# Kernel optimization log

Hardware: AMD Instinct MI355X
Metric: run time of the kernel (lower is better)

## Reference

```python
import jax, jax.numpy as jnp
import numpy as np

E, B, T, DIN, D = 8, 16, 512, 256, 256  # ensemble, batch, seq, input_dim, d_model*factor


def setup_inputs() -> dict:
    key = jax.random.key(0)
    ks = jax.random.split(key, 9)
    s_in = 1.0 / np.sqrt(DIN)
    s_d = 1.0 / np.sqrt(D)
    return {
        "x": jax.random.normal(ks[0], (E, B, T, DIN), jnp.float32),
        "hidden": jnp.zeros((1, E * B, 2 * D), jnp.float32),
        "rnn_start": (jax.random.uniform(ks[1], (B, T, 1)) < 0.02).astype(jnp.float32),
        "W_in": jax.random.normal(ks[2], (2, E, DIN, D), jnp.float32) * s_in,
        "b_in": jax.random.normal(ks[3], (2, E, D), jnp.float32) * 0.01,
        "W_mid": jax.random.normal(ks[4], (4, E, D, D), jnp.float32) * s_d,
        "b_mid": jax.random.normal(ks[5], (4, E, D), jnp.float32) * 0.01,
        "W_out": jax.random.normal(ks[6], (E, D, D), jnp.float32) * s_d,
        "b_out": jax.random.normal(ks[7], (E, D), jnp.float32) * 0.01,
    }


def _scan_tie_input_gate(v, f, h0):
    # h_t = f_t * h_{t-1} + (1 - f_t) * v_t  (tied input gate), via associative scan.
    # v, f: [N, T, D]; h0: [N, 1, D]
    b = (1.0 - f) * v

    def combine(x, y):
        a1, b1 = x
        a2, b2 = y
        return a1 * a2, a2 * b1 + b2

    A, Bc = jax.lax.associative_scan(combine, (f, b), axis=1)
    out = A * h0 + Bc  # [N, T, D]
    return out, out[:, -1:, :]


def reference(x, hidden, rnn_start, W_in, b_in, W_mid, b_mid, W_out, b_out):
    # --- first GILR stage ---
    u = jnp.einsum('ebti,meio->mebto', x, W_in) + b_in[:, :, None, None, :]
    v = jnp.tanh(u[0])
    f = jax.nn.sigmoid(u[1])
    f = f * (1.0 - rnn_start)[None]  # rnn_start [B,T,1] broadcasts over E, D

    vr = v.reshape(E * B, T, D)
    fr = f.reshape(E * B, T, D)

    h_pre, h_mid = jnp.split(hidden, 2, axis=-1)          # each [1, E*B, D]
    h_pre = jnp.transpose(h_pre, (1, 0, 2))               # [E*B, 1, D]
    h_mid = jnp.transpose(h_mid, (1, 0, 2))

    vr, h_pre_last = _scan_tie_input_gate(vr, fr, h_pre)
    v4 = vr.reshape(E, B, T, D)

    # --- LSTM-like middle stage ---
    u = jnp.einsum('ebti,meio->mebto', v4, W_mid) + b_mid[:, :, None, None, :]
    f = jax.nn.sigmoid(u[0])
    i = jax.nn.sigmoid(u[1])
    o = jax.nn.sigmoid(u[2])
    z = jnp.tanh(u[3])
    f = f * (1.0 - rnn_start)[None]

    fr = f.reshape(E * B, T, D)
    izr = (i * z).reshape(E * B, T, D)
    orr = o.reshape(E * B, T, D)

    out, h_mid_last = _scan_tie_input_gate(izr, fr, h_mid)
    out = out * orr
    out4 = out.reshape(E, B, T, D)

    # --- output projection ---
    out4 = jnp.einsum('ebti,eio->ebto', out4, W_out) + b_out[:, None, None, :]

    hidden_out = jnp.transpose(jnp.concatenate([h_pre_last, h_mid_last], axis=-1), (1, 0, 2))
    return out4, hidden_out
```

## Files before the change

### kernel.cpp

```cpp
#include <hip/hip_runtime.h>
#include <hip/hip_bf16.h>
#include <stdint.h>
#include <stddef.h>


typedef __bf16 bf16x8 __attribute__((ext_vector_type(8)));
typedef __bf16 bf16x4 __attribute__((ext_vector_type(4)));
typedef __bf16 bf16x2 __attribute__((ext_vector_type(2)));
typedef float  f32x4  __attribute__((ext_vector_type(4)));
typedef float  f32x2  __attribute__((ext_vector_type(2)));

#define E_ 8
#define M_ 8192
#define K_ 256

__device__ __forceinline__ float sigm_f(float x) {
    return __builtin_amdgcn_rcpf(1.0f + __expf(-x));
}
__device__ __forceinline__ float tanh_f(float x) {
    return 1.0f - 2.0f * __builtin_amdgcn_rcpf(1.0f + __expf(2.0f * x));
}

__device__ __forceinline__ void g2lds16(const void* g, void* l) {
    __builtin_amdgcn_global_load_lds((const __attribute__((address_space(1))) void*)g,
                                     (__attribute__((address_space(3))) void*)l, 16, 0, 0);
}

template <int D>
__device__ __forceinline__ float dppshr(float x) {
    return __builtin_bit_cast(float,
        __builtin_amdgcn_update_dpp(0, __builtin_bit_cast(int, x),
                                    0x110 | D, 0xF, 0xF, true));
}

__device__ __forceinline__ void lane_scan(float& A, float& B, float& EA, float& EB, int ln15) {
    float As, Bs;
    Bs = dppshr<1>(B); As = dppshr<1>(A); B = __builtin_fmaf(A, Bs, B); A = (ln15 >= 1) ? A * As : A;
    Bs = dppshr<2>(B); As = dppshr<2>(A); B = __builtin_fmaf(A, Bs, B); A = (ln15 >= 2) ? A * As : A;
    Bs = dppshr<4>(B); As = dppshr<4>(A); B = __builtin_fmaf(A, Bs, B); A = (ln15 >= 4) ? A * As : A;
    Bs = dppshr<8>(B); As = dppshr<8>(A); B = __builtin_fmaf(A, Bs, B); A = (ln15 >= 8) ? A * As : A;
    EA = dppshr<1>(A); EA = (ln15 >= 1) ? EA : 1.0f;
    EB = dppshr<1>(B);
}

__global__ __launch_bounds__(256) void transw_all(const float* __restrict__ W_in,
                                                  const float* __restrict__ W_mid,
                                                  const float* __restrict__ W_out,
                                                  __bf16* __restrict__ Wt1,
                                                  __bf16* __restrict__ Wt2,
                                                  __bf16* __restrict__ Wt3) {
    int z = blockIdx.z;
    const float* src; __bf16* dst; int NG, ilv, ge;
    if (z < 16)      { src = W_in;  dst = Wt1; NG = 2; ilv = 1; ge = z; }
    else if (z < 48) { src = W_mid; dst = Wt2; NG = 4; ilv = 1; ge = z - 16; }
    else             { src = W_out; dst = Wt3; NG = 1; ilv = 0; ge = z - 48; }
    int g = ge >> 3, e = ge & 7;
    int k0 = blockIdx.x * 64, d0 = blockIdx.y * 64;
    __shared__ float tile[64][65];
    int t = threadIdx.x;
#pragma unroll
    for (int j = 0; j < 16; ++j) {
        int lin = j * 256 + t;
        int r = lin >> 6, c = lin & 63;
        tile[r][c] = src[((size_t)(ge * 256 + k0 + r)) * 256 + d0 + c];
    }
    __syncthreads();
#pragma unroll
    for (int j = 0; j < 16; ++j) {
        int lin = j * 256 + t;
        int r = lin >> 6, c = lin & 63;
        int d = d0 + r;
        int row = ilv ? (d * NG + g) : (g * 256 + d);
        dst[((size_t)(e * NG * 256 + row)) * K_ + k0 + c] = (__bf16)tile[c][r];
    }
}

template <int MODE, int NG>
__global__ __launch_bounds__(512, 1) void gemm_k(const __bf16* __restrict__ A,
                                                 const float* __restrict__ Af,
                                                 const __bf16* __restrict__ Wt,
                                                 const float* __restrict__ bias,
                                                 const float* __restrict__ rs,
                                                 __bf16* __restrict__ gout,
                                                 float* __restrict__ fout,
                                                 const float* __restrict__ hidden,
                                                 float* __restrict__ hidout) {
    constexpr int NT  = NG * 2;
    constexpr int NMT = 2 * NT;
    const int tid = threadIdx.x;
    const int bid = blockIdx.x;
    const int e  = bid & 7;
    const int rr = bid >> 3;
    const int nt = rr & (NT - 1);
    const int ms = rr / NT;
    const int mt0 = ms * NMT;
    const int lane = tid & 63, wid = tid >> 6;
    const int wr = wid >> 2, wc = wid & 3;
    const int ln15 = lane & 15, ln16 = lane >> 4;

    __shared__ __align__(16) __bf16 As[2][32768];
    __shared__ float cAl[64], cBl[64];
    __shared__ float chL[2][64];

    bf16x8 Breg[2][8];
    {
        const __bf16* bp = Wt + ((size_t)e * (NG * 256) + nt * 128 + wc * 32 + ln15) * K_ + ln16 * 8;
#pragma unroll
        for (int j = 0; j < 2; ++j)
#pragma unroll
            for (int s = 0; s < 8; ++s)
                Breg[j][s] = *(const bf16x8*)(bp + (size_t)j * 16 * K_ + s * 32);
    }
    f32x4 bias_v[2];
#pragma unroll
    for (int j = 0; j < 2; ++j) {
        int n0 = nt * 128 + wc * 32 + j * 16 + (ln16 << 2);
        if constexpr (MODE == 0) {
#pragma unroll
            for (int q = 0; q < 4; ++q) {
                int n = n0 + q;
                bias_v[j][q] = bias[((n & 1) * E_ + e) * 256 + (n >> 1)];
            }
        } else if constexpr (MODE == 1) {
#pragma unroll
            for (int q = 0; q < 4; ++q) {
                int n = n0 + q;
                bias_v[j][q] = bias[((n & 3) * E_ + e) * 256 + (n >> 2)];
            }
        } else {
            bias_v[j] = *(const f32x4*)&bias[e * 256 + n0];
        }
    }

    const int sr = tid >> 5, sr2 = sr >> 2;
    const int gg0 = (tid & 31) ^ sr2;
    const size_t Aoff = ((size_t)e * M_ + (size_t)mt0 * 128) * K_;
    const __bf16* sE = nullptr; const __bf16* sO = nullptr;
    const float*  sEf = nullptr; const float* sOf = nullptr;
    if constexpr (MODE == 0) {
        sEf = Af + Aoff + (size_t)sr * K_ + gg0 * 8;
        sOf = Af + Aoff + (size_t)sr * K_ + (gg0 ^ 4) * 8;
    } else {
        sE = A + Aoff + (size_t)sr * K_ + gg0 * 8;
        sO = A + Aoff + (size_t)sr * K_ + (gg0 ^ 4) * 8;
    }
    __bf16* const dbase0 = &As[0][tid * 8];
    __bf16* const dbase1 = &As[1][tid * 8];

    auto stage = [&](int tt, int buf) {
        __bf16* d = buf ? dbase1 : dbase0;
        const size_t toff = (size_t)tt * (128 * K_);
#pragma unroll
        for (int q = 0; q < 8; ++q)
            g2lds16(((q & 1) ? sO : sE) + toff + q * (16 * K_), d + q * 4096);
    };

    f32x4 tA[8], tB[8];
    auto loadx = [&](int tt) {
        const size_t toff = (size_t)tt * (128 * K_);
#pragma unroll
        for (int q = 0; q < 8; ++q) {
            const float* s = ((q & 1) ? sOf : sEf) + toff + q * (16 * K_);
            tA[q] = *(const f32x4*)s;
            tB[q] = *(const f32x4*)(s + 4);
        }
    };
    auto writex = [&](int buf) {
        __bf16* d = buf ? dbase1 : dbase0;
#pragma unroll
        for (int q = 0; q < 8; ++q) {
            bf16x8 w;
#pragma unroll
            for (int k = 0; k < 4; ++k) { w[k] = (__bf16)tA[q][k]; w[4 + k] = (__bf16)tB[q][k]; }
            *(bf16x8*)(d + q * 4096) = w;
        }
    };

    const int rowb = (wr * 64 + ln15 * 4) * K_;
    const int gb = ln16 ^ (lane & 7);
    const int pe_off = rowb + gb * 8;
    const int po_off = rowb + (gb ^ 4) * 8;

    auto compute = [&](f32x4 (&acc)[4][2], int buf) {
        const __bf16* pe = &As[0][0] + buf * 32768 + pe_off;
        const __bf16* po = &As[0][0] + buf * 32768 + po_off;
#pragma unroll
        for (int s = 0; s < 8; ++s) {
            const __bf16* p = (s & 1) ? po : pe;
            bf16x8 af[4];
#pragma unroll
            for (int i = 0; i < 4; ++i)
                af[i] = *(const bf16x8*)(p + i * K_ + (s >> 1) * 64);
#pragma unroll
            for (int i = 0; i < 4; ++i)
#pragma unroll
                for (int j = 0; j < 2; ++j)
                    acc[i][j] = __builtin_amdgcn_mfma_f32_16x16x32_bf16(Breg[j][s], af[i], acc[i][j], 0, 0, 0);
        }
    };

    if constexpr (MODE == 2) {
        stage(0, 0);
        asm volatile("s_waitcnt vmcnt(0)" ::: "memory");
        __builtin_amdgcn_s_barrier();
        __builtin_amdgcn_sched_barrier(0);
        f32x4 acc[4][2] = {};
        int buf = 0;
        for (int t = 0; t < NMT; ++t) {
            if (t + 1 < NMT) stage(t + 1, buf ^ 1);
            compute(acc, buf);
            const int mb = (mt0 + t) * 128 + wr * 64 + ln15 * 4;
#pragma unroll
            for (int j = 0; j < 2; ++j) {
                const int n0 = nt * 128 + wc * 32 + j * 16 + (ln16 << 2);
#pragma unroll
                for (int i = 0; i < 4; ++i) {
                    f32x4 o = acc[i][j] + bias_v[j];
                    *(f32x4*)&fout[((size_t)e * M_ + mb + i) * 256 + n0] = o;
                    acc[i][j] = f32x4{};
                }
            }
            asm volatile("s_waitcnt vmcnt(8) lgkmcnt(0)" ::: "memory");
            __builtin_amdgcn_s_barrier();
            __builtin_amdgcn_sched_barrier(0);
            buf ^= 1;
        }
        return;
    } else {
        auto do_epi = [&](f32x4 (&acc)[4][2], int tp, const f32x4& rs4p, const float* hidvp) {
            const bool cs = ((tp & 3) == 0);
            const int c = tp >> 2;
            const int mb = (mt0 + tp) * 128 + wr * 64 + ln15 * 4;
            f32x4 rsv;
#pragma unroll
            for (int q = 0; q < 4; ++q) rsv[q] = 1.0f - rs4p[q];

            if constexpr (MODE == 1) {
                float PA[2][4], PB[2][4], Ov[2][4], LA[2], LB[2], EA[2], EB[2];
#pragma unroll
                for (int j = 0; j < 2; ++j) {
#pragma unroll
                    for (int i = 0; i < 4; ++i) {
                        float f  = sigm_f(acc[i][j][0] + bias_v[j][0]) * rsv[i];
                        float iv = sigm_f(acc[i][j][1] + bias_v[j][1]);
                        float o  = sigm_f(acc[i][j][2] + bias_v[j][2]);
                        float z  = tanh_f(acc[i][j][3] + bias_v[j][3]);
                        float b  = (1.0f - f) * iv * z;
                        Ov[j][i] = o;
                        if (i == 0) { PA[j][0] = f; PB[j][0] = b; }
                        else { PB[j][i] = __builtin_fmaf(f, PB[j][i - 1], b); PA[j][i] = PA[j][i - 1] * f; }
                        acc[i][j] = f32x4{};
                    }
                    LA[j] = PA[j][3]; LB[j] = PB[j][3];
                    lane_scan(LA[j], LB[j], EA[j], EB[j], ln15);
                }
                if (wr == 0 && ln15 == 15) {
#pragma unroll
                    for (int j = 0; j < 2; ++j) {
                        int sl = wc * 8 + j * 4 + ln16;
                        cAl[sl] = LA[j]; cBl[sl] = LB[j];
                    }
                }
                asm volatile("s_waitcnt lgkmcnt(0)" ::: "memory");
                __builtin_amdgcn_s_barrier();
#pragma unroll
                for (int j = 0; j < 2; ++j) {
                    const int sl = wc * 8 + j * 4 + ln16;
                    const int d = nt * 32 + wc * 8 + j * 4 + ln16;
                    float hp = cs ? hidvp[j] : chL[tp & 1][sl];
                    float hs = wr ? __builtin_fmaf(cAl[sl], hp, cBl[sl]) : hp;
                    float h0 = __builtin_fmaf(EA[j], hs, EB[j]);
#pragma unroll
                    for (int i = 0; i < 4; ++i) {
                        float h = __builtin_fmaf(PA[j][i], h0, PB[j][i]);
                        gout[((size_t)e * M_ + mb + i) * 256 + d] = (__bf16)(h * Ov[j][i]);
                    }
                    if (wr == 1 && ln15 == 15) {
                        float he = __builtin_fmaf(LA[j], hs, LB[j]);
                        chL[(tp + 1) & 1][sl] = he;
                        if ((tp & 3) == 3)
                            hidout[(e * 16 + ms * 4 + c) * 512 + 256 + d] = he;
                    }
                }
            } else {
                float PA[2][2][4], PB[2][2][4], LA[2][2], LB[2][2], EA[2][2], EB[2][2];
#pragma unroll
                for (int j = 0; j < 2; ++j) {
#pragma unroll
                    for (int dq = 0; dq < 2; ++dq) {
#pragma unroll
                        for (int i = 0; i < 4; ++i) {
                            float uv = acc[i][j][dq * 2 + 0] + bias_v[j][dq * 2 + 0];
                            float uf = acc[i][j][dq * 2 + 1] + bias_v[j][dq * 2 + 1];
                            float f = sigm_f(uf) * rsv[i];
                            float b = (1.0f - f) * tanh_f(uv);
                            if (i == 0) { PA[j][dq][0] = f; PB[j][dq][0] = b; }
                            else { PB[j][dq][i] = __builtin_fmaf(f, PB[j][dq][i - 1], b);
                                   PA[j][dq][i] = PA[j][dq][i - 1] * f; }
                        }
                        LA[j][dq] = PA[j][dq][3]; LB[j][dq] = PB[j][dq][3];
                        lane_scan(LA[j][dq], LB[j][dq], EA[j][dq], EB[j][dq], ln15);
                    }
#pragma unroll
                    for (int i = 0; i < 4; ++i) acc[i][j] = f32x4{};
                }
                if (wr == 0 && ln15 == 15) {
#pragma unroll
                    for (int j = 0; j < 2; ++j)
#pragma unroll
                        for (int dq = 0; dq < 2; ++dq) {
                            int sl = wc * 16 + j * 8 + ln16 * 2 + dq;
                            cAl[sl] = LA[j][dq]; cBl[sl] = LB[j][dq];
                        }
                }
                asm volatile("s_waitcnt lgkmcnt(0)" ::: "memory");
                __builtin_amdgcn_s_barrier();
#pragma unroll
                for (int j = 0; j < 2; ++j) {
                    const int D0 = nt * 64 + wc * 16 + j * 8 + ln16 * 2;
                    float h0q[2];
#pragma unroll
                    for (int dq = 0; dq < 2; ++dq) {
                        const int sl = wc * 16 + j * 8 + ln16 * 2 + dq;
                        float hp = cs ? hidvp[j * 2 + dq] : chL[tp & 1][sl];
                        float hs = wr ? __builtin_fmaf(cAl[sl], hp, cBl[sl]) : hp;
                        h0q[dq] = __builtin_fmaf(EA[j][dq], hs, EB[j][dq]);
                        if (wr == 1 && ln15 == 15) {
                            float he = __builtin_fmaf(LA[j][dq], hs, LB[j][dq]);
                            chL[(tp + 1) & 1][sl] = he;
                            if ((tp & 3) == 3)
                                hidout[(e * 16 + ms * 2 + c) * 512 + D0 + dq] = he;
                        }
                    }
#pragma unroll
                    for (int i = 0; i < 4; ++i) {
                        float ha = __builtin_fmaf(PA[j][0][i], h0q[0], PB[j][0][i]);
                        float hb = __builtin_fmaf(PA[j][1][i], h0q[1], PB[j][1][i]);
                        bf16x2 pk; pk[0] = (__bf16)ha; pk[1] = (__bf16)hb;
                        *(unsigned int*)&gout[((size_t)e * M_ + mb + i) * 256 + D0] =
                            __builtin_bit_cast(unsigned int, pk);
                    }
                }
            }
        };

        if constexpr (MODE == 0) {
            loadx(0);
            asm volatile("s_waitcnt vmcnt(0)" ::: "memory");
            writex(0);
            asm volatile("s_waitcnt lgkmcnt(0)" ::: "memory");
        } else {
            stage(0, 0);
            asm volatile("s_waitcnt vmcnt(0)" ::: "memory");
        }
        __builtin_amdgcn_s_barrier();
        __builtin_amdgcn_sched_barrier(0);

        f32x4 accA[4][2] = {}, accB[4][2] = {};
        f32x4 rs4_p = {};
        float hidv_p[4] = {0.f, 0.f, 0.f, 0.f};
        int buf = 0;

        auto iter = [&](int t, f32x4 (&accC)[4][2], f32x4 (&accP)[4][2]) {
            const int c = t >> 2;
            f32x4 rs4_n;
            float hidv_n[4] = {0.f, 0.f, 0.f, 0.f};
            {
                const int mbh = (mt0 + t) * 128 + wr * 64 + ln15 * 4;
                rs4_n = *(const f32x4*)&rs[mbh];
                if constexpr (MODE == 1) {
                    const int nrow = e * 16 + ms * 4 + c;
                    hidv_n[0] = hidden[nrow * 512 + 256 + (nt * 32 + wc * 8 + 0 + ln16)];
                    hidv_n[1] = hidden[nrow * 512 + 256 + (nt * 32 + wc * 8 + 4 + ln16)];
                } else {
                    const int nrow = e * 16 + ms * 2 + c;
                    f32x2 ha = *(const f32x2*)&hidden[nrow * 512 + (nt * 64 + wc * 16 + 0 + ln16 * 2)];
                    f32x2 hb = *(const f32x2*)&hidden[nrow * 512 + (nt * 64 + wc * 16 + 8 + ln16 * 2)];
                    hidv_n[0] = ha[0]; hidv_n[1] = ha[1]; hidv_n[2] = hb[0]; hidv_n[3] = hb[1];
                }
                __builtin_amdgcn_sched_barrier(0);
            }
            if constexpr (MODE == 0) {
                if (t + 1 < NMT) loadx(t + 1);
                __builtin_amdgcn_sched_barrier(0);
            } else {
                if (t + 1 < NMT) stage(t + 1, buf ^ 1);
            }
            compute(accC, buf);
            if (t > 0) do_epi(accP, t - 1, rs4_p, hidv_p);
            if (t == 0) {
                asm volatile("s_waitcnt vmcnt(0)" ::: "memory");
            } else {
                asm volatile("s_waitcnt vmcnt(8)" ::: "memory");
            }
            if constexpr (MODE == 0) {
                if (t + 1 < NMT) writex(buf ^ 1);
            }
            asm volatile("s_waitcnt lgkmcnt(0)" ::: "memory");
            __builtin_amdgcn_s_barrier();
            __builtin_amdgcn_sched_barrier(0);
            buf ^= 1;
            rs4_p = rs4_n;
#pragma unroll
            for (int q = 0; q < 4; ++q) hidv_p[q] = hidv_n[q];
        };

#pragma unroll 1
        for (int t2 = 0; t2 < NMT; t2 += 2) {
            iter(t2, accA, accB);
            iter(t2 + 1, accB, accA);
        }
        do_epi(accB, NMT - 1, rs4_p, hidv_p);
    }
}

extern "C" void kernel_launch(void* const* d_in, const int* in_sizes, int n_in,
                              void* d_out, int out_size, void* d_ws, size_t ws_size,
                              hipStream_t stream) {
    const float* x      = (const float*)d_in[0];
    const float* hidden = (const float*)d_in[1];
    const float* rs     = (const float*)d_in[2];
    const float* W_in   = (const float*)d_in[3];
    const float* b_in   = (const float*)d_in[4];
    const float* W_mid  = (const float*)d_in[5];
    const float* b_mid  = (const float*)d_in[6];
    const float* W_out  = (const float*)d_in[7];
    const float* b_out  = (const float*)d_in[8];
    float* out = (float*)d_out;

    char* ws = (char*)d_ws;
    const size_t MiB = (size_t)1 << 20;
    __bf16* Wt1 = (__bf16*)(ws + 0);
    __bf16* Wt2 = (__bf16*)(ws + 2 * MiB);
    __bf16* Wt3 = (__bf16*)(ws + 6 * MiB);
    __bf16* v4b = (__bf16*)(ws + 8 * MiB);
    __bf16* G   = (__bf16*)(ws + 72 * MiB);

    float* hidout = out + (size_t)E_ * M_ * 256;

    transw_all<<<dim3(4, 4, 56), 256, 0, stream>>>(W_in, W_mid, W_out, Wt1, Wt2, Wt3);

    gemm_k<0, 2><<<256, 512, 0, stream>>>(nullptr, x, Wt1, b_in, rs, v4b, nullptr, hidden, hidout);
    gemm_k<1, 4><<<256, 512, 0, stream>>>(v4b, nullptr, Wt2, b_mid, rs, G, nullptr, hidden, hidout);
    gemm_k<2, 1><<<256, 512, 0, stream>>>(G, nullptr, Wt3, b_out, nullptr, nullptr, out, nullptr, nullptr);
}
```

Before: 162.3 us.

## Split GEMM stages into dedicated kernels with per-wave LDS-free tiling

The templated gemm kernel is split into three kernels. Stage 1 keeps the original LDS-staged pipeline. Stages 2 and 3 become LDS-free kernels where each wave loads A fragments directly from global memory into registers and launches many more smaller blocks (1024 and 2048 blocks of 256 threads). In stage 2 each wave owns a whole sequence for one column group and carries the scan state across time tiles with a cross-lane permute, removing the block-level barrier and LDS carry exchange. The trade is direct global loads with no double buffering in exchange for higher occupancy and no synchronisation.

```diff
diff --git a/kernel.cpp b/kernel.cpp
--- a/kernel.cpp
+++ b/kernel.cpp
@@ -75,18 +75,15 @@
     }
 }
 
-template <int MODE, int NG>
-__global__ __launch_bounds__(512, 1) void gemm_k(const __bf16* __restrict__ A,
-                                                 const float* __restrict__ Af,
-                                                 const __bf16* __restrict__ Wt,
-                                                 const float* __restrict__ bias,
-                                                 const float* __restrict__ rs,
-                                                 __bf16* __restrict__ gout,
-                                                 float* __restrict__ fout,
-                                                 const float* __restrict__ hidden,
-                                                 float* __restrict__ hidout) {
-    constexpr int NT  = NG * 2;
-    constexpr int NMT = 2 * NT;
+__global__ __launch_bounds__(512, 1) void gemm1_k(const float* __restrict__ Af,
+                                                  const __bf16* __restrict__ Wt,
+                                                  const float* __restrict__ bias,
+                                                  const float* __restrict__ rs,
+                                                  __bf16* __restrict__ gout,
+                                                  const float* __restrict__ hidden,
+                                                  float* __restrict__ hidout) {
+    constexpr int NT  = 4;
+    constexpr int NMT = 8;
     const int tid = threadIdx.x;
     const int bid = blockIdx.x;
     const int e  = bid & 7;
@@ -104,7 +101,7 @@
 
     bf16x8 Breg[2][8];
     {
-        const __bf16* bp = Wt + ((size_t)e * (NG * 256) + nt * 128 + wc * 32 + ln15) * K_ + ln16 * 8;
+        const __bf16* bp = Wt + ((size_t)e * 512 + nt * 128 + wc * 32 + ln15) * K_ + ln16 * 8;
 #pragma unroll
         for (int j = 0; j < 2; ++j)
 #pragma unroll
@@ -113,47 +110,20 @@
     }
     f32x4 bias_v[2];
 #pragma unroll
-    for (int j = 0; j < 2; ++j) {
-        int n0 = nt * 128 + wc * 32 + j * 16 + (ln16 << 2);
-        if constexpr (MODE == 0) {
-#pragma unroll
-            for (int q = 0; q < 4; ++q) {
-                int n = n0 + q;
-                bias_v[j][q] = bias[((n & 1) * E_ + e) * 256 + (n >> 1)];
-            }
-        } else if constexpr (MODE == 1) {
-#pragma unroll
-            for (int q = 0; q < 4; ++q) {
-                int n = n0 + q;
-                bias_v[j][q] = bias[((n & 3) * E_ + e) * 256 + (n >> 2)];
-            }
-        } else {
-            bias_v[j] = *(const f32x4*)&bias[e * 256 + n0];
-        }
-    }
+    for (int j = 0; j < 2; ++j)
+#pragma unroll
+        for (int q = 0; q < 4; ++q) {
+            int n = nt * 128 + wc * 32 + j * 16 + (ln16 << 2) + q;
+            bias_v[j][q] = bias[((n & 1) * E_ + e) * 256 + (n >> 1)];
+        }
 
     const int sr = tid >> 5, sr2 = sr >> 2;
     const int gg0 = (tid & 31) ^ sr2;
     const size_t Aoff = ((size_t)e * M_ + (size_t)mt0 * 128) * K_;
-    const __bf16* sE = nullptr; const __bf16* sO = nullptr;
-    const float*  sEf = nullptr; const float* sOf = nullptr;
-    if constexpr (MODE == 0) {
-        sEf = Af + Aoff + (size_t)sr * K_ + gg0 * 8;
-        sOf = Af + Aoff + (size_t)sr * K_ + (gg0 ^ 4) * 8;
-    } else {
-        sE = A + Aoff + (size_t)sr * K_ + gg0 * 8;
-        sO = A + Aoff + (size_t)sr * K_ + (gg0 ^ 4) * 8;
-    }
+    const float* sEf = Af + Aoff + (size_t)sr * K_ + gg0 * 8;
+    const float* sOf = Af + Aoff + (size_t)sr * K_ + (gg0 ^ 4) * 8;
     __bf16* const dbase0 = &As[0][tid * 8];
     __bf16* const dbase1 = &As[1][tid * 8];
-
-    auto stage = [&](int tt, int buf) {
-        __bf16* d = buf ? dbase1 : dbase0;
-        const size_t toff = (size_t)tt * (128 * K_);
-#pragma unroll
-        for (int q = 0; q < 8; ++q)
-            g2lds16(((q & 1) ? sO : sE) + toff + q * (16 * K_), d + q * 4096);
-    };
 
     f32x4 tA[8], tB[8];
     auto loadx = [&](int tt) {
@@ -199,218 +169,268 @@
         }
     };
 
-    if constexpr (MODE == 2) {
-        stage(0, 0);
-        asm volatile("s_waitcnt vmcnt(0)" ::: "memory");
+    auto do_epi = [&](f32x4 (&acc)[4][2], int tp, const f32x4& rs4p, const float* hidvp) {
+        const bool cs = ((tp & 3) == 0);
+        const int c = tp >> 2;
+        const int mb = (mt0 + tp) * 128 + wr * 64 + ln15 * 4;
+        f32x4 rsv;
+#pragma unroll
+        for (int q = 0; q < 4; ++q) rsv[q] = 1.0f - rs4p[q];
+        float PA[2][2][4], PB[2][2][4], LA[2][2], LB[2][2], EA[2][2], EB[2][2];
+#pragma unroll
+        for (int j = 0; j < 2; ++j) {
+#pragma unroll
+            for (int dq = 0; dq < 2; ++dq) {
+#pragma unroll
+                for (int i = 0; i < 4; ++i) {
+                    float uv = acc[i][j][dq * 2 + 0] + bias_v[j][dq * 2 + 0];
+                    float uf = acc[i][j][dq * 2 + 1] + bias_v[j][dq * 2 + 1];
+                    float f = sigm_f(uf) * rsv[i];
+                    float b = (1.0f - f) * tanh_f(uv);
+                    if (i == 0) { PA[j][dq][0] = f; PB[j][dq][0] = b; }
+                    else { PB[j][dq][i] = __builtin_fmaf(f, PB[j][dq][i - 1], b);
+                           PA[j][dq][i] = PA[j][dq][i - 1] * f; }
+                }
+                LA[j][dq] = PA[j][dq][3]; LB[j][dq] = PB[j][dq][3];
+                lane_scan(LA[j][dq], LB[j][dq], EA[j][dq], EB[j][dq], ln15);
+            }
+#pragma unroll
+            for (int i = 0; i < 4; ++i) acc[i][j] = f32x4{};
+        }
+        if (wr == 0 && ln15 == 15) {
+#pragma unroll
+            for (int j = 0; j < 2; ++j)
+#pragma unroll
+                for (int dq = 0; dq < 2; ++dq) {
+                    int sl = wc * 16 + j * 8 + ln16 * 2 + dq;
+                    cAl[sl] = LA[j][dq]; cBl[sl] = LB[j][dq];
+                }
+        }
+        asm volatile("s_waitcnt lgkmcnt(0)" ::: "memory");
+        __builtin_amdgcn_s_barrier();
+#pragma unroll
+        for (int j = 0; j < 2; ++j) {
+            const int D0 = nt * 64 + wc * 16 + j * 8 + ln16 * 2;
+            float h0q[2];
+#pragma unroll
+            for (int dq = 0; dq < 2; ++dq) {
+                const int sl = wc * 16 + j * 8 + ln16 * 2 + dq;
+                float hp = cs ? hidvp[j * 2 + dq] : chL[tp & 1][sl];
+                float hsv = wr ? __builtin_fmaf(cAl[sl], hp, cBl[sl]) : hp;
+                h0q[dq] = __builtin_fmaf(EA[j][dq], hsv, EB[j][dq]);
+                if (wr == 1 && ln15 == 15) {
+                    float he = __builtin_fmaf(LA[j][dq], hsv, LB[j][dq]);
+                    chL[(tp + 1) & 1][sl] = he;
+                    if ((tp & 3) == 3)
+                        hidout[(e * 16 + ms * 2 + c) * 512 + D0 + dq] = he;
+                }
+            }
+#pragma unroll
+            for (int i = 0; i < 4; ++i) {
+                float ha = __builtin_fmaf(PA[j][0][i], h0q[0], PB[j][0][i]);
+                float hb = __builtin_fmaf(PA[j][1][i], h0q[1], PB[j][1][i]);
+                bf16x2 pk; pk[0] = (__bf16)ha; pk[1] = (__bf16)hb;
+                *(unsigned int*)&gout[((size_t)e * M_ + mb + i) * 256 + D0] =
+                    __builtin_bit_cast(unsigned int, pk);
+            }
+        }
+    };
+
+    loadx(0);
+    asm volatile("s_waitcnt vmcnt(0)" ::: "memory");
+    writex(0);
+    asm volatile("s_waitcnt lgkmcnt(0)" ::: "memory");
+    __builtin_amdgcn_s_barrier();
+    __builtin_amdgcn_sched_barrier(0);
+
+    f32x4 accA[4][2] = {}, accB[4][2] = {};
+    f32x4 rs4_p = {};
+    float hidv_p[4] = {0.f, 0.f, 0.f, 0.f};
+    int buf = 0;
+
+    auto iter = [&](int t, f32x4 (&accC)[4][2], f32x4 (&accP)[4][2]) {
+        const int c = t >> 2;
+        f32x4 rs4_n;
+        float hidv_n[4];
+        {
+            const int mbh = (mt0 + t) * 128 + wr * 64 + ln15 * 4;
+            rs4_n = *(const f32x4*)&rs[mbh];
+            const int nrow = e * 16 + ms * 2 + c;
+            f32x2 ha = *(const f32x2*)&hidden[nrow * 512 + (nt * 64 + wc * 16 + 0 + ln16 * 2)];
+            f32x2 hb = *(const f32x2*)&hidden[nrow * 512 + (nt * 64 + wc * 16 + 8 + ln16 * 2)];
+            hidv_n[0] = ha[0]; hidv_n[1] = ha[1]; hidv_n[2] = hb[0]; hidv_n[3] = hb[1];
+            __builtin_amdgcn_sched_barrier(0);
+        }
+        if (t + 1 < NMT) loadx(t + 1);
+        __builtin_amdgcn_sched_barrier(0);
+        compute(accC, buf);
+        if (t > 0) do_epi(accP, t - 1, rs4_p, hidv_p);
+        if (t == 0) { asm volatile("s_waitcnt vmcnt(0)" ::: "memory"); }
+        else        { asm volatile("s_waitcnt vmcnt(8)" ::: "memory"); }
+        if (t + 1 < NMT) writex(buf ^ 1);
+        asm volatile("s_waitcnt lgkmcnt(0)" ::: "memory");
         __builtin_amdgcn_s_barrier();
         __builtin_amdgcn_sched_barrier(0);
+        buf ^= 1;
+        rs4_p = rs4_n;
+#pragma unroll
+        for (int q = 0; q < 4; ++q) hidv_p[q] = hidv_n[q];
+    };
+
+#pragma unroll 1
+    for (int t2 = 0; t2 < NMT; t2 += 2) {
+        iter(t2, accA, accB);
+        iter(t2 + 1, accB, accA);
+    }
+    do_epi(accB, NMT - 1, rs4_p, hidv_p);
+}
+
+__global__ __launch_bounds__(256) void gemm2_k(const __bf16* __restrict__ A,
+                                               const __bf16* __restrict__ Wt,
+                                               const float* __restrict__ bias,
+                                               const float* __restrict__ rs,
+                                               __bf16* __restrict__ G,
+                                               const float* __restrict__ hidden,
+                                               float* __restrict__ hidout) {
+    const int tid = threadIdx.x;
+    const int lane = tid & 63, wid = tid >> 6;
+    const int bid = blockIdx.x;
+    const int e = bid & 7;
+    const int wk = (bid >> 3) * 4 + wid;
+    const int cg = wk >> 4;
+    const int b  = wk & 15;
+    const int ln15 = lane & 15, ln16 = lane >> 4;
+
+    bf16x8 Breg[2][8];
+    {
+        const __bf16* bp = Wt + ((size_t)e * 1024 + cg * 32 + ln15) * K_ + ln16 * 8;
+#pragma unroll
+        for (int j = 0; j < 2; ++j)
+#pragma unroll
+            for (int s = 0; s < 8; ++s)
+                Breg[j][s] = *(const bf16x8*)(bp + (size_t)j * 16 * K_ + s * 32);
+    }
+    f32x4 bias_v[2];
+#pragma unroll
+    for (int j = 0; j < 2; ++j)
+#pragma unroll
+        for (int q = 0; q < 4; ++q) {
+            int n = cg * 32 + j * 16 + (ln16 << 2) + q;
+            bias_v[j][q] = bias[((n & 3) * E_ + e) * 256 + (n >> 2)];
+        }
+
+    const size_t Ab = ((size_t)e * M_ + (size_t)b * 512) * K_;
+    const __bf16* ap = A + Ab + (size_t)(ln15 * 4) * K_ + ln16 * 8;
+    const int d0 = cg * 8 + ln16;
+    float hs[2];
+    hs[0] = hidden[(e * 16 + b) * 512 + 256 + d0];
+    hs[1] = hidden[(e * 16 + b) * 512 + 256 + d0 + 4];
+    const int bpa = (lane | 15) << 2;
+
+#pragma unroll 1
+    for (int t = 0; t < 8; ++t) {
+        const int mb = b * 512 + t * 64 + ln15 * 4;
+        f32x4 rs4 = *(const f32x4*)&rs[mb];
+        const __bf16* at = ap + (size_t)t * (64 * K_);
         f32x4 acc[4][2] = {};
-        int buf = 0;
-        for (int t = 0; t < NMT; ++t) {
-            if (t + 1 < NMT) stage(t + 1, buf ^ 1);
-            compute(acc, buf);
-            const int mb = (mt0 + t) * 128 + wr * 64 + ln15 * 4;
-#pragma unroll
-            for (int j = 0; j < 2; ++j) {
-                const int n0 = nt * 128 + wc * 32 + j * 16 + (ln16 << 2);
-#pragma unroll
-                for (int i = 0; i < 4; ++i) {
-                    f32x4 o = acc[i][j] + bias_v[j];
-                    *(f32x4*)&fout[((size_t)e * M_ + mb + i) * 256 + n0] = o;
-                    acc[i][j] = f32x4{};
-                }
-            }
-            asm volatile("s_waitcnt vmcnt(8) lgkmcnt(0)" ::: "memory");
-            __builtin_amdgcn_s_barrier();
-            __builtin_amdgcn_sched_barrier(0);
-            buf ^= 1;
-        }
-        return;
-    } else {
-        auto do_epi = [&](f32x4 (&acc)[4][2], int tp, const f32x4& rs4p, const float* hidvp) {
-            const bool cs = ((tp & 3) == 0);
-            const int c = tp >> 2;
-            const int mb = (mt0 + tp) * 128 + wr * 64 + ln15 * 4;
-            f32x4 rsv;
-#pragma unroll
-            for (int q = 0; q < 4; ++q) rsv[q] = 1.0f - rs4p[q];
-
-            if constexpr (MODE == 1) {
-                float PA[2][4], PB[2][4], Ov[2][4], LA[2], LB[2], EA[2], EB[2];
-#pragma unroll
-                for (int j = 0; j < 2; ++j) {
-#pragma unroll
-                    for (int i = 0; i < 4; ++i) {
-                        float f  = sigm_f(acc[i][j][0] + bias_v[j][0]) * rsv[i];
-                        float iv = sigm_f(acc[i][j][1] + bias_v[j][1]);
-                        float o  = sigm_f(acc[i][j][2] + bias_v[j][2]);
-                        float z  = tanh_f(acc[i][j][3] + bias_v[j][3]);
-                        float b  = (1.0f - f) * iv * z;
-                        Ov[j][i] = o;
-                        if (i == 0) { PA[j][0] = f; PB[j][0] = b; }
-                        else { PB[j][i] = __builtin_fmaf(f, PB[j][i - 1], b); PA[j][i] = PA[j][i - 1] * f; }
-                        acc[i][j] = f32x4{};
-                    }
-                    LA[j] = PA[j][3]; LB[j] = PB[j][3];
-                    lane_scan(LA[j], LB[j], EA[j], EB[j], ln15);
-                }
-                if (wr == 0 && ln15 == 15) {
-#pragma unroll
-                    for (int j = 0; j < 2; ++j) {
-                        int sl = wc * 8 + j * 4 + ln16;
-                        cAl[sl] = LA[j]; cBl[sl] = LB[j];
-                    }
-                }
-                asm volatile("s_waitcnt lgkmcnt(0)" ::: "memory");
-                __builtin_amdgcn_s_barrier();
-#pragma unroll
-                for (int j = 0; j < 2; ++j) {
-                    const int sl = wc * 8 + j * 4 + ln16;
-                    const int d = nt * 32 + wc * 8 + j * 4 + ln16;
-                    float hp = cs ? hidvp[j] : chL[tp & 1][sl];
-                    float hs = wr ? __builtin_fmaf(cAl[sl], hp, cBl[sl]) : hp;
-                    float h0 = __builtin_fmaf(EA[j], hs, EB[j]);
-#pragma unroll
-                    for (int i = 0; i < 4; ++i) {
-                        float h = __builtin_fmaf(PA[j][i], h0, PB[j][i]);
-                        gout[((size_t)e * M_ + mb + i) * 256 + d] = (__bf16)(h * Ov[j][i]);
-                    }
-                    if (wr == 1 && ln15 == 15) {
-                        float he = __builtin_fmaf(LA[j], hs, LB[j]);
-                        chL[(tp + 1) & 1][sl] = he;
-                        if ((tp & 3) == 3)
-                            hidout[(e * 16 + ms * 4 + c) * 512 + 256 + d] = he;
-                    }
-                }
-            } else {
-                float PA[2][2][4], PB[2][2][4], LA[2][2], LB[2][2], EA[2][2], EB[2][2];
-#pragma unroll
-                for (int j = 0; j < 2; ++j) {
-#pragma unroll
-                    for (int dq = 0; dq < 2; ++dq) {
-#pragma unroll
-                        for (int i = 0; i < 4; ++i) {
-                            float uv = acc[i][j][dq * 2 + 0] + bias_v[j][dq * 2 + 0];
-                            float uf = acc[i][j][dq * 2 + 1] + bias_v[j][dq * 2 + 1];
-                            float f = sigm_f(uf) * rsv[i];
-                            float b = (1.0f - f) * tanh_f(uv);
-                            if (i == 0) { PA[j][dq][0] = f; PB[j][dq][0] = b; }
-                            else { PB[j][dq][i] = __builtin_fmaf(f, PB[j][dq][i - 1], b);
-                                   PA[j][dq][i] = PA[j][dq][i - 1] * f; }
-                        }
-                        LA[j][dq] = PA[j][dq][3]; LB[j][dq] = PB[j][dq][3];
-                        lane_scan(LA[j][dq], LB[j][dq], EA[j][dq], EB[j][dq], ln15);
-                    }
-#pragma unroll
-                    for (int i = 0; i < 4; ++i) acc[i][j] = f32x4{};
-                }
-                if (wr == 0 && ln15 == 15) {
-#pragma unroll
-                    for (int j = 0; j < 2; ++j)
-#pragma unroll
-                        for (int dq = 0; dq < 2; ++dq) {
-                            int sl = wc * 16 + j * 8 + ln16 * 2 + dq;
-                            cAl[sl] = LA[j][dq]; cBl[sl] = LB[j][dq];
-                        }
-                }
-                asm volatile("s_waitcnt lgkmcnt(0)" ::: "memory");
-                __builtin_amdgcn_s_barrier();
-#pragma unroll
-                for (int j = 0; j < 2; ++j) {
-                    const int D0 = nt * 64 + wc * 16 + j * 8 + ln16 * 2;
-                    float h0q[2];
-#pragma unroll
-                    for (int dq = 0; dq < 2; ++dq) {
-                        const int sl = wc * 16 + j * 8 + ln16 * 2 + dq;
-                        float hp = cs ? hidvp[j * 2 + dq] : chL[tp & 1][sl];
-                        float hs = wr ? __builtin_fmaf(cAl[sl], hp, cBl[sl]) : hp;
-                        h0q[dq] = __builtin_fmaf(EA[j][dq], hs, EB[j][dq]);
-                        if (wr == 1 && ln15 == 15) {
-                            float he = __builtin_fmaf(LA[j][dq], hs, LB[j][dq]);
-                            chL[(tp + 1) & 1][sl] = he;
-                            if ((tp & 3) == 3)
-                                hidout[(e * 16 + ms * 2 + c) * 512 + D0 + dq] = he;
-                        }
-                    }
-#pragma unroll
-                    for (int i = 0; i < 4; ++i) {
-                        float ha = __builtin_fmaf(PA[j][0][i], h0q[0], PB[j][0][i]);
-                        float hb = __builtin_fmaf(PA[j][1][i], h0q[1], PB[j][1][i]);
-                        bf16x2 pk; pk[0] = (__bf16)ha; pk[1] = (__bf16)hb;
-                        *(unsigned int*)&gout[((size_t)e * M_ + mb + i) * 256 + D0] =
-                            __builtin_bit_cast(unsigned int, pk);
-                    }
-                }
-            }
-        };
-
-        if constexpr (MODE == 0) {
-            loadx(0);
-            asm volatile("s_waitcnt vmcnt(0)" ::: "memory");
-            writex(0);
-            asm volatile("s_waitcnt lgkmcnt(0)" ::: "memory");
-        } else {
-            stage(0, 0);
-            asm volatile("s_waitcnt vmcnt(0)" ::: "memory");
-        }
-        __builtin_amdgcn_s_barrier();
-        __builtin_amdgcn_sched_barrier(0);
-
-        f32x4 accA[4][2] = {}, accB[4][2] = {};
-        f32x4 rs4_p = {};
-        float hidv_p[4] = {0.f, 0.f, 0.f, 0.f};
-        int buf = 0;
-
-        auto iter = [&](int t, f32x4 (&accC)[4][2], f32x4 (&accP)[4][2]) {
-            const int c = t >> 2;
-            f32x4 rs4_n;
-            float hidv_n[4] = {0.f, 0.f, 0.f, 0.f};
-            {
-                const int mbh = (mt0 + t) * 128 + wr * 64 + ln15 * 4;
-                rs4_n = *(const f32x4*)&rs[mbh];
-                if constexpr (MODE == 1) {
-                    const int nrow = e * 16 + ms * 4 + c;
-                    hidv_n[0] = hidden[nrow * 512 + 256 + (nt * 32 + wc * 8 + 0 + ln16)];
-                    hidv_n[1] = hidden[nrow * 512 + 256 + (nt * 32 + wc * 8 + 4 + ln16)];
-                } else {
-                    const int nrow = e * 16 + ms * 2 + c;
-                    f32x2 ha = *(const f32x2*)&hidden[nrow * 512 + (nt * 64 + wc * 16 + 0 + ln16 * 2)];
-                    f32x2 hb = *(const f32x2*)&hidden[nrow * 512 + (nt * 64 + wc * 16 + 8 + ln16 * 2)];
-                    hidv_n[0] = ha[0]; hidv_n[1] = ha[1]; hidv_n[2] = hb[0]; hidv_n[3] = hb[1];
-                }
-                __builtin_amdgcn_sched_barrier(0);
-            }
-            if constexpr (MODE == 0) {
-                if (t + 1 < NMT) loadx(t + 1);
-                __builtin_amdgcn_sched_barrier(0);
-            } else {
-                if (t + 1 < NMT) stage(t + 1, buf ^ 1);
-            }
-            compute(accC, buf);
-            if (t > 0) do_epi(accP, t - 1, rs4_p, hidv_p);
-            if (t == 0) {
-                asm volatile("s_waitcnt vmcnt(0)" ::: "memory");
-            } else {
-                asm volatile("s_waitcnt vmcnt(8)" ::: "memory");
-            }
-            if constexpr (MODE == 0) {
-                if (t + 1 < NMT) writex(buf ^ 1);
-            }
-            asm volatile("s_waitcnt lgkmcnt(0)" ::: "memory");
-            __builtin_amdgcn_s_barrier();
-            __builtin_amdgcn_sched_barrier(0);
-            buf ^= 1;
-            rs4_p = rs4_n;
-#pragma unroll
-            for (int q = 0; q < 4; ++q) hidv_p[q] = hidv_n[q];
-        };
-
-#pragma unroll 1
-        for (int t2 = 0; t2 < NMT; t2 += 2) {
-            iter(t2, accA, accB);
-            iter(t2 + 1, accB, accA);
-        }
-        do_epi(accB, NMT - 1, rs4_p, hidv_p);
+#pragma unroll
+        for (int s = 0; s < 8; ++s) {
+            bf16x8 af[4];
+#pragma unroll
+            for (int i = 0; i < 4; ++i)
+                af[i] = *(const bf16x8*)(at + i * K_ + s * 32);
+#pragma unroll
+            for (int i = 0; i < 4; ++i) {
+                acc[i][0] = __builtin_amdgcn_mfma_f32_16x16x32_bf16(Breg[0][s], af[i], acc[i][0], 0, 0, 0);
+                acc[i][1] = __builtin_amdgcn_mfma_f32_16x16x32_bf16(Breg[1][s], af[i], acc[i][1], 0, 0, 0);
+            }
+        }
+        f32x4 rsv;
+#pragma unroll
+        for (int q = 0; q < 4; ++q) rsv[q] = 1.0f - rs4[q];
+#pragma unroll
+        for (int j = 0; j < 2; ++j) {
+            float PA[4], PB[4], Ov[4];
+#pragma unroll
+            for (int i = 0; i < 4; ++i) {
+                float f  = sigm_f(acc[i][j][0] + bias_v[j][0]) * rsv[i];
+                float iv = sigm_f(acc[i][j][1] + bias_v[j][1]);
+                float o  = sigm_f(acc[i][j][2] + bias_v[j][2]);
+                float z  = tanh_f(acc[i][j][3] + bias_v[j][3]);
+                float bb = (1.0f - f) * iv * z;
+                Ov[i] = o;
+                PA[i] = i ? PA[i - 1] * f : f;
+                PB[i] = i ? __builtin_fmaf(f, PB[i - 1], bb) : bb;
+            }
+            float LA = PA[3], LB = PB[3], EA, EB;
+            lane_scan(LA, LB, EA, EB, ln15);
+            float h0 = __builtin_fmaf(EA, hs[j], EB);
+            const int d = d0 + j * 4;
+#pragma unroll
+            for (int i = 0; i < 4; ++i) {
+                float h = __builtin_fmaf(PA[i], h0, PB[i]);
+                G[((size_t)e * M_ + mb + i) * 256 + d] = (__bf16)(h * Ov[i]);
+            }
+            float hn = __builtin_fmaf(LA, hs[j], LB);
+            hn = __builtin_bit_cast(float,
+                 __builtin_amdgcn_ds_bpermute(bpa, __builtin_bit_cast(int, hn)));
+            hs[j] = hn;
+            if (t == 7 && ln15 == 15)
+                hidout[(e * 16 + b) * 512 + 256 + d] = hn;
+        }
+    }
+}
+
+__global__ __launch_bounds__(256) void gemm3_k(const __bf16* __restrict__ A,
+                                               const __bf16* __restrict__ Wt,
+                                               const float* __restrict__ bias,
+                                               float* __restrict__ out) {
+    const int tid = threadIdx.x;
+    const int lane = tid & 63, wid = tid >> 6;
+    const int bid = blockIdx.x;
+    const int e = bid & 7;
+    const int wk = (bid >> 3) * 4 + wid;
+    const int cg = wk >> 7;
+    const int mt = wk & 127;
+    const int ln15 = lane & 15, ln16 = lane >> 4;
+
+    bf16x8 Breg[2][8];
+    {
+        const __bf16* bp = Wt + ((size_t)e * 256 + cg * 32 + ln15) * K_ + ln16 * 8;
+#pragma unroll
+        for (int j = 0; j < 2; ++j)
+#pragma unroll
+            for (int s = 0; s < 8; ++s)
+                Breg[j][s] = *(const bf16x8*)(bp + (size_t)j * 16 * K_ + s * 32);
+    }
+    f32x4 bias_v[2];
+#pragma unroll
+    for (int j = 0; j < 2; ++j)
+        bias_v[j] = *(const f32x4*)&bias[e * 256 + cg * 32 + j * 16 + (ln16 << 2)];
+
+    const __bf16* at = A + ((size_t)e * M_ + mt * 64 + ln15 * 4) * K_ + ln16 * 8;
+    f32x4 acc[4][2] = {};
+#pragma unroll
+    for (int s = 0; s < 8; ++s) {
+        bf16x8 af[4];
+#pragma unroll
+        for (int i = 0; i < 4; ++i)
+            af[i] = *(const bf16x8*)(at + i * K_ + s * 32);
+#pragma unroll
+        for (int i = 0; i < 4; ++i) {
+            acc[i][0] = __builtin_amdgcn_mfma_f32_16x16x32_bf16(Breg[0][s], af[i], acc[i][0], 0, 0, 0);
+            acc[i][1] = __builtin_amdgcn_mfma_f32_16x16x32_bf16(Breg[1][s], af[i], acc[i][1], 0, 0, 0);
+        }
+    }
+    const int mb = mt * 64 + ln15 * 4;
+#pragma unroll
+    for (int j = 0; j < 2; ++j) {
+        const int n0 = cg * 32 + j * 16 + (ln16 << 2);
+#pragma unroll
+        for (int i = 0; i < 4; ++i) {
+            f32x4 o = acc[i][j] + bias_v[j];
+            *(f32x4*)&out[((size_t)e * M_ + mb + i) * 256 + n0] = o;
+        }
     }
 }
 
@@ -440,7 +460,7 @@
 
     transw_all<<<dim3(4, 4, 56), 256, 0, stream>>>(W_in, W_mid, W_out, Wt1, Wt2, Wt3);
 
-    gemm_k<0, 2><<<256, 512, 0, stream>>>(nullptr, x, Wt1, b_in, rs, v4b, nullptr, hidden, hidout);
-    gemm_k<1, 4><<<256, 512, 0, stream>>>(v4b, nullptr, Wt2, b_mid, rs, G, nullptr, hidden, hidout);
-    gemm_k<2, 1><<<256, 512, 0, stream>>>(G, nullptr, Wt3, b_out, nullptr, nullptr, out, nullptr, nullptr);
-}
+    gemm1_k<<<256, 512, 0, stream>>>(x, Wt1, b_in, rs, v4b, hidden, hidout);
+    gemm2_k<<<1024, 256, 0, stream>>>(v4b, Wt2, b_mid, rs, G, hidden, hidout);
+    gemm3_k<<<2048, 256, 0, stream>>>(G, Wt3, b_out, out);
+}
```

Measured after the change: 262.3 us. 1.62x slower.
